# Performance work log

Measured on AMD Instinct MI355X. Metric: run time of the kernel, lower is better.

The kernel has to match this reference:

```python
import jax, jax.numpy as jnp
import numpy as np

NUM_EMBEDDINGS = 1024
EMBEDDING_DIM = 64
COMMITMENT_COST = 0.25


def setup_inputs() -> dict:
    key = jax.random.key(0)
    k1, k2 = jax.random.split(key)
    inputs = jax.random.normal(k1, (32, 64, 64, 64), dtype=jnp.float32)
    # embedding initialized uniform(-1/K, 1/K), matching the torch init
    emb = jax.random.uniform(k2, (NUM_EMBEDDINGS, EMBEDDING_DIM), dtype=jnp.float32,
                             minval=-1.0 / NUM_EMBEDDINGS, maxval=1.0 / NUM_EMBEDDINGS)
    return {"inputs": inputs, "emb": emb}


def reference(inputs, emb):
    K, D = emb.shape
    flat = inputs.reshape(-1, D)                     # [N, D]
    distances = (jnp.sum(flat * flat, axis=1, keepdims=True)
                 + jnp.sum(emb * emb, axis=1)
                 - 2.0 * flat @ emb.T)
    encoding_indices = jnp.argmin(distances, axis=1)  # [N]
    # gather (same math as one-hot @ emb, without materializing [N, K] one-hot)
    quantized = emb[encoding_indices].reshape(inputs.shape)
    # straight-through estimator
    quantized_st = inputs + jax.lax.stop_gradient(quantized - inputs)
    e_latent_loss = jnp.mean((jax.lax.stop_gradient(quantized_st) - inputs) ** 2)
    q_latent_loss = jnp.mean((quantized_st - jax.lax.stop_gradient(inputs)) ** 2)
    loss = q_latent_loss + COMMITMENT_COST * e_latent_loss
    # codebook usage stats (mean of one-hot == normalized histogram of indices)
    N = flat.shape[0]
    counts = jnp.zeros((K,), dtype=jnp.float32).at[encoding_indices].add(1.0)
    avg_probs = counts / N
    perplexity = jnp.exp(-jnp.sum(avg_probs * jnp.log(avg_probs + 1e-10)))
    return quantized_st, loss, perplexity
```

## Files before the change

kernel.cpp:

```cpp
#include <hip/hip_runtime.h>
#include <hip/hip_fp16.h>
#include <float.h>

#define N_ROWS   131072
#define DIM      64
#define NCODES   1024
#define MB       256
#define TPB      1024
#define NCHUNK   16
#define NBLK     (N_ROWS / MB)

typedef __attribute__((ext_vector_type(8))) short short8;
typedef __attribute__((ext_vector_type(4))) float floatx4;


__device__ inline ushort f2h(float f) { return __half_as_ushort(__float2half_rn(f)); }

__device__ inline uint swz(uint row, uint b) { return row * 128u + (b ^ ((row & 7u) << 4)); }

__global__ void vq_prep(const float* __restrict__ emb, float* __restrict__ nh,
                        int* __restrict__ counts8, ushort* __restrict__ blob) {
    int g = blockIdx.x * 256 + threadIdx.x;
    int l = g & 63;
    int l15 = l & 15, lhi = l >> 4;
    int c = g >> 8, q = (g >> 6) & 3;
    int code = c * 64 + q * 16 + l15;
    int k0 = lhi * 8;
    const float* er = emb + (size_t)code * DIM;

    ushort tmp[16];
    #pragma unroll
    for (int j = 0; j < 8; ++j) {
        tmp[j]     = f2h(er[k0 + j]      * 1024.0f);
        tmp[8 + j] = f2h(er[32 + k0 + j] * 1024.0f);
    }
    ushort* dst = blob + (size_t)g * 16;
    *(short8*)(dst)     = *(const short8*)(tmp);
    *(short8*)(dst + 8) = *(const short8*)(tmp + 8);

    counts8[2 * g]     = 0;
    counts8[2 * g + 1] = 0;

    if (g < NCODES) {
        float s = 0.f;
        const float* e = emb + (size_t)g * DIM;
        #pragma unroll
        for (int d = 0; d < DIM; ++d) s += e[d] * e[d];
        nh[g] = 64.0f - 512.0f * s;
    }
}

__global__ __launch_bounds__(TPB, 4) void vq_main(
        const float* __restrict__ x, const float* __restrict__ emb,
        const ushort* __restrict__ blob, const float* __restrict__ nh,
        float* __restrict__ out, int* __restrict__ counts8, float* __restrict__ ssePart) {

    __shared__ __align__(16) ushort xh[MB * DIM];
    __shared__ uint  part1[MB][4];
    __shared__ int   rowIdx[MB];
    __shared__ float wred[16];

    const int tid = threadIdx.x;
    const int lane = tid & 63;
    const int w = tid >> 6;
    const int wq = w & 3;
    const int rowQ = (w >> 2) * 64;
    const int l15 = lane & 15, lhi = lane >> 4;
    const int rowBase = blockIdx.x * MB;

    #pragma unroll
    for (int i = 0; i < 4; ++i) {
        int f = tid + TPB * i; int r = f >> 4, d4 = f & 15;
        float4 v = ((const float4*)x)[(size_t)(rowBase + r) * 16 + d4];
        ushort4 h = make_ushort4(f2h(v.x), f2h(v.y), f2h(v.z), f2h(v.w));
        *(ushort4*)((char*)xh + swz((uint)r, (uint)d4 * 8u)) = h;
    }
    __syncthreads();

    short8 afr[4][2];
    #pragma unroll
    for (int rm = 0; rm < 4; ++rm)
        #pragma unroll
        for (int ks = 0; ks < 2; ++ks)
            afr[rm][ks] = *(const short8*)((char*)xh + swz((uint)(rowQ + rm * 16 + l15),
                                                           (uint)(ks * 64 + lhi * 16)));

    uint keys[16];
    #pragma unroll
    for (int s = 0; s < 16; ++s) keys[s] = 0u;

    const int codeBase = wq * 16 + l15;
    const ushort* bp = blob + ((size_t)wq * 64 + lane) * 16;

    auto body = [&](short8 f0, short8 f1, float nhv, uint invc) {
        floatx4 acc[4];
        #pragma unroll
        for (int rm = 0; rm < 4; ++rm) acc[rm] = (floatx4){nhv, nhv, nhv, nhv};
        #pragma unroll
        for (int rm = 0; rm < 4; ++rm) {
            acc[rm] = __builtin_amdgcn_mfma_f32_16x16x32_f16(afr[rm][0], f0, acc[rm], 0, 0, 0);
            acc[rm] = __builtin_amdgcn_mfma_f32_16x16x32_f16(afr[rm][1], f1, acc[rm], 0, 0, 0);
        }
        #pragma unroll
        for (int rm = 0; rm < 4; ++rm)
            #pragma unroll
            for (int j = 0; j < 4; ++j) {
                uint kb = (__float_as_uint(acc[rm][j]) & 0xFFFFFC00u) | invc;
                int s = rm * 4 + j;
                keys[s] = keys[s] > kb ? keys[s] : kb;
            }
    };

    short8 cur0 = *(const short8*)(bp);
    short8 cur1 = *(const short8*)(bp + 8);
    float  nhc  = nh[codeBase];
    uint   invc = 1023u - (uint)codeBase;

    #pragma unroll 1
    for (int c = 0; c < NCHUNK - 1; ++c) {
        const ushort* np_ = bp + (size_t)(c + 1) * 4096;
        short8 nxt0 = *(const short8*)(np_);
        short8 nxt1 = *(const short8*)(np_ + 8);
        float  nhn  = nh[(c + 1) * 64 + codeBase];

        body(cur0, cur1, nhc, invc);

        cur0 = nxt0; cur1 = nxt1; nhc = nhn; invc -= 64u;
    }
    body(cur0, cur1, nhc, invc);

    #pragma unroll
    for (int s = 0; s < 16; ++s) {
        uint k = keys[s];
        #pragma unroll
        for (int m = 1; m < 16; m <<= 1) {
            uint ok = __shfl_xor(k, m);
            k = ok > k ? ok : k;
        }
        if (l15 == 0)
            part1[rowQ + (s >> 2) * 16 + lhi * 4 + (s & 3)][wq] = k;
    }
    __syncthreads();

    if (tid < MB) {
        uint p = part1[tid][0];
        #pragma unroll
        for (int g = 1; g < 4; ++g) {
            uint q = part1[tid][g];
            p = q > p ? q : p;
        }
        int code = 1023 - (int)(p & 1023u);
        rowIdx[tid] = code;
        atomicAdd(&counts8[(blockIdx.x & 7) * NCODES + code], 1);
    }
    __syncthreads();

    float myss = 0.f;
    #pragma unroll
    for (int i = 0; i < 4; ++i) {
        int f = tid + TPB * i; int r = f >> 4, d4 = f & 15;
        int idx = rowIdx[r];
        float4 q  = ((const float4*)emb)[(size_t)idx * 16 + d4];
        float4 xv = ((const float4*)x)[(size_t)(rowBase + r) * 16 + d4];
        float4 o;
        o.x = xv.x + (q.x - xv.x);
        o.y = xv.y + (q.y - xv.y);
        o.z = xv.z + (q.z - xv.z);
        o.w = xv.w + (q.w - xv.w);
        ((float4*)out)[(size_t)(rowBase + r) * 16 + d4] = o;
        float gx = o.x - xv.x, gy = o.y - xv.y, gz = o.z - xv.z, gw = o.w - xv.w;
        myss += gx * gx + gy * gy + gz * gz + gw * gw;
    }
    #pragma unroll
    for (int m = 32; m >= 1; m >>= 1) myss += __shfl_down(myss, m);
    if (lane == 0) wred[w] = myss;
    __syncthreads();
    if (tid == 0) {
        float s = 0.f;
        #pragma unroll
        for (int i = 0; i < 16; ++i) s += wred[i];
        ssePart[blockIdx.x] = s;
    }
}

__global__ void vq_final(const int* __restrict__ counts8, const float* __restrict__ ssePart,
                         float* __restrict__ out) {
    __shared__ float pe[16], ps[16];
    int k = threadIdx.x;
    int cnt = 0;
    #pragma unroll
    for (int s = 0; s < 8; ++s) cnt += counts8[s * NCODES + k];
    float p = (float)cnt * (1.0f / (float)N_ROWS);
    float ent = p * logf(p + 1e-10f);
    float sp = (k < NBLK) ? ssePart[k] : 0.0f;
    #pragma unroll
    for (int m = 32; m >= 1; m >>= 1) {
        ent += __shfl_down(ent, m);
        sp  += __shfl_down(sp, m);
    }
    if ((k & 63) == 0) { pe[k >> 6] = ent; ps[k >> 6] = sp; }
    __syncthreads();
    if (k == 0) {
        float es = 0.f, ss = 0.f;
        #pragma unroll
        for (int w = 0; w < 16; ++w) { es += pe[w]; ss += ps[w]; }
        out[(size_t)N_ROWS * DIM]     = 1.25f * (ss / (float)(N_ROWS * DIM));
        out[(size_t)N_ROWS * DIM + 1] = expf(-es);
    }
}

extern "C" void kernel_launch(void* const* d_in, const int* in_sizes, int n_in,
                              void* d_out, int out_size, void* d_ws, size_t ws_size,
                              hipStream_t stream) {
    const float* x   = (const float*)d_in[0];
    const float* emb = (const float*)d_in[1];
    float*  out     = (float*)d_out;
    float*  nh      = (float*)d_ws;
    int*    counts8 = (int*)((char*)d_ws + 4096);
    float*  ssePrt  = (float*)((char*)d_ws + 36864);
    ushort* blob    = (ushort*)((char*)d_ws + 40960);

    vq_prep<<<16, 256, 0, stream>>>(emb, nh, counts8, blob);
    vq_main<<<NBLK, TPB, 0, stream>>>(x, emb, blob, nh, out, counts8, ssePrt);
    vq_final<<<1, 1024, 0, stream>>>(counts8, ssePrt, out);
}
```

Baseline: 50.68 us.

## Load MFMA A-fragments directly from global and halve block size

Each block now covers 128 rows with 512 threads instead of 256 rows with 1024. The x tile is no longer staged through swizzled LDS: each lane loads its MFMA A-fragments straight from global memory and converts them to fp16. The rowIdx buffer and one barrier are dropped because every consumer recomputes the argmin from part1. Per-wave SSE partials go straight to global and vq_final sums eight per thread. This cuts LDS use and barriers to allow more resident blocks, at the cost of strided, less coalesced global loads and a redundant argmin recompute per element.

```diff
diff --git a/kernel.cpp b/kernel.cpp
--- a/kernel.cpp
+++ b/kernel.cpp
@@ -5,8 +5,8 @@
 #define N_ROWS   131072
 #define DIM      64
 #define NCODES   1024
-#define MB       256
-#define TPB      1024
+#define MB       128
+#define TPB      512
 #define NCHUNK   16
 #define NBLK     (N_ROWS / MB)
 
@@ -15,8 +15,6 @@
 
 
 __device__ inline ushort f2h(float f) { return __half_as_ushort(__float2half_rn(f)); }
-
-__device__ inline uint swz(uint row, uint b) { return row * 128u + (b ^ ((row & 7u) << 4)); }
 
 __global__ void vq_prep(const float* __restrict__ emb, float* __restrict__ nh,
                         int* __restrict__ counts8, ushort* __restrict__ blob) {
@@ -50,15 +48,12 @@
     }
 }
 
-__global__ __launch_bounds__(TPB, 4) void vq_main(
+__global__ __launch_bounds__(TPB, 3) void vq_main(
         const float* __restrict__ x, const float* __restrict__ emb,
         const ushort* __restrict__ blob, const float* __restrict__ nh,
         float* __restrict__ out, int* __restrict__ counts8, float* __restrict__ ssePart) {
 
-    __shared__ __align__(16) ushort xh[MB * DIM];
-    __shared__ uint  part1[MB][4];
-    __shared__ int   rowIdx[MB];
-    __shared__ float wred[16];
+    __shared__ __align__(16) uint part1[MB][4];
 
     const int tid = threadIdx.x;
     const int lane = tid & 63;
@@ -68,22 +63,24 @@
     const int l15 = lane & 15, lhi = lane >> 4;
     const int rowBase = blockIdx.x * MB;
 
-    #pragma unroll
-    for (int i = 0; i < 4; ++i) {
-        int f = tid + TPB * i; int r = f >> 4, d4 = f & 15;
-        float4 v = ((const float4*)x)[(size_t)(rowBase + r) * 16 + d4];
-        ushort4 h = make_ushort4(f2h(v.x), f2h(v.y), f2h(v.z), f2h(v.w));
-        *(ushort4*)((char*)xh + swz((uint)r, (uint)d4 * 8u)) = h;
-    }
-    __syncthreads();
-
     short8 afr[4][2];
-    #pragma unroll
-    for (int rm = 0; rm < 4; ++rm)
-        #pragma unroll
-        for (int ks = 0; ks < 2; ++ks)
-            afr[rm][ks] = *(const short8*)((char*)xh + swz((uint)(rowQ + rm * 16 + l15),
-                                                           (uint)(ks * 64 + lhi * 16)));
+    {
+        const float* xb = x + (size_t)(rowBase + rowQ) * DIM;
+        #pragma unroll
+        for (int rm = 0; rm < 4; ++rm)
+            #pragma unroll
+            for (int ks = 0; ks < 2; ++ks) {
+                const float* p = xb + (size_t)(rm * 16 + l15) * DIM + ks * 32 + lhi * 8;
+                float4 a = *(const float4*)(p);
+                float4 b = *(const float4*)(p + 4);
+                short8 v;
+                v[0] = (short)f2h(a.x); v[1] = (short)f2h(a.y);
+                v[2] = (short)f2h(a.z); v[3] = (short)f2h(a.w);
+                v[4] = (short)f2h(b.x); v[5] = (short)f2h(b.y);
+                v[6] = (short)f2h(b.z); v[7] = (short)f2h(b.w);
+                afr[rm][ks] = v;
+            }
+    }
 
     uint keys[16];
     #pragma unroll
@@ -143,23 +140,22 @@
     __syncthreads();
 
     if (tid < MB) {
-        uint p = part1[tid][0];
-        #pragma unroll
-        for (int g = 1; g < 4; ++g) {
-            uint q = part1[tid][g];
-            p = q > p ? q : p;
-        }
-        int code = 1023 - (int)(p & 1023u);
-        rowIdx[tid] = code;
-        atomicAdd(&counts8[(blockIdx.x & 7) * NCODES + code], 1);
-    }
-    __syncthreads();
+        uint4 pv = *(const uint4*)&part1[tid][0];
+        uint m01 = pv.x > pv.y ? pv.x : pv.y;
+        uint m23 = pv.z > pv.w ? pv.z : pv.w;
+        uint m = m01 > m23 ? m01 : m23;
+        atomicAdd(&counts8[(blockIdx.x & 7) * NCODES + (1023 - (int)(m & 1023u))], 1);
+    }
 
     float myss = 0.f;
     #pragma unroll
     for (int i = 0; i < 4; ++i) {
         int f = tid + TPB * i; int r = f >> 4, d4 = f & 15;
-        int idx = rowIdx[r];
+        uint4 pv = *(const uint4*)&part1[r][0];
+        uint m01 = pv.x > pv.y ? pv.x : pv.y;
+        uint m23 = pv.z > pv.w ? pv.z : pv.w;
+        uint m = m01 > m23 ? m01 : m23;
+        int idx = 1023 - (int)(m & 1023u);
         float4 q  = ((const float4*)emb)[(size_t)idx * 16 + d4];
         float4 xv = ((const float4*)x)[(size_t)(rowBase + r) * 16 + d4];
         float4 o;
@@ -173,14 +169,7 @@
     }
     #pragma unroll
     for (int m = 32; m >= 1; m >>= 1) myss += __shfl_down(myss, m);
-    if (lane == 0) wred[w] = myss;
-    __syncthreads();
-    if (tid == 0) {
-        float s = 0.f;
-        #pragma unroll
-        for (int i = 0; i < 16; ++i) s += wred[i];
-        ssePart[blockIdx.x] = s;
-    }
+    if (lane == 0) ssePart[blockIdx.x * 8 + w] = myss;
 }
 
 __global__ void vq_final(const int* __restrict__ counts8, const float* __restrict__ ssePart,
@@ -192,7 +181,9 @@
     for (int s = 0; s < 8; ++s) cnt += counts8[s * NCODES + k];
     float p = (float)cnt * (1.0f / (float)N_ROWS);
     float ent = p * logf(p + 1e-10f);
-    float sp = (k < NBLK) ? ssePart[k] : 0.0f;
+    float sp = 0.f;
+    #pragma unroll
+    for (int s = 0; s < 8; ++s) sp += ssePart[k * 8 + s];
     #pragma unroll
     for (int m = 32; m >= 1; m >>= 1) {
         ent += __shfl_down(ent, m);
@@ -218,7 +209,7 @@
     float*  nh      = (float*)d_ws;
     int*    counts8 = (int*)((char*)d_ws + 4096);
     float*  ssePrt  = (float*)((char*)d_ws + 36864);
-    ushort* blob    = (ushort*)((char*)d_ws + 40960);
+    ushort* blob    = (ushort*)((char*)d_ws + 69632);
 
     vq_prep<<<16, 256, 0, stream>>>(emb, nh, counts8, blob);
     vq_main<<<NBLK, TPB, 0, stream>>>(x, emb, blob, nh, out, counts8, ssePrt);
```

Result: slower. 53.29 us (+5.2%).
